# Performance work log

Measured on AMD Instinct MI355X. Metric: run time of the kernel, lower is better.

Reference implementation:

```python
import jax, jax.numpy as jnp
import numpy as np

NA, NB = 4096, 4096
IN, H, E = 256, 512, 131072
NEG_SLOPE = 0.2


def setup_inputs() -> dict:
    key = jax.random.key(0)
    ks = jax.random.split(key, 32)
    f32 = jnp.float32
    nrm = lambda k, s, sc=0.05: jax.random.normal(k, s, f32) * sc
    inp = {
        'x_A': jax.random.normal(ks[0], (NA, IN), f32),
        'x_B': jax.random.normal(ks[1], (NB, IN), f32),
        'edge_AB': jax.random.randint(ks[2], (2, E), 0, NA, jnp.int32),
        'edge_BA': jax.random.randint(ks[3], (2, E), 0, NB, jnp.int32),
        'W_inA': nrm(ks[4], (H, IN)), 'b_inA': jnp.zeros((H,), f32),
        'W_inB': nrm(ks[5], (H, IN)), 'b_inB': jnp.zeros((H,), f32),
        'W_in2A': nrm(ks[6], (H, IN)), 'b_in2A': jnp.zeros((H,), f32),
        'W_in2B': nrm(ks[7], (H, IN)), 'b_in2B': jnp.zeros((H,), f32),
        'Wg1': nrm(ks[8], (H, H)), 'a_src1': nrm(ks[9], (H,)),
        'a_dst1': nrm(ks[10], (H,)), 'bg1': jnp.zeros((H,), f32),
        'Wg2': nrm(ks[11], (H, H)), 'a_src2': nrm(ks[12], (H,)),
        'a_dst2': nrm(ks[13], (H,)), 'bg2': jnp.zeros((H,), f32),
        'Wqkv': nrm(ks[14], (3 * H, H)), 'bqkv': jnp.zeros((3 * H,), f32),
        'Wo': nrm(ks[15], (H, H)), 'bo': jnp.zeros((H,), f32),
    }
    return inp


def gat_conv(x, src, dst, W, a_src, a_dst, b, n):
    # PyG GATConv, heads=1: linear transform, per-edge additive attention,
    # LeakyReLU + segment softmax over incoming edges of each dst node,
    # scatter-sum of weighted source messages. Self-loops already in src/dst.
    h = x @ W.T                                # [n, H]
    e = jax.nn.leaky_relu((h @ a_src)[src] + (h @ a_dst)[dst], NEG_SLOPE)
    m = jax.ops.segment_max(e, dst, num_segments=n)
    ex = jnp.exp(e - m[dst])
    denom = jax.ops.segment_sum(ex, dst, num_segments=n)
    alpha = ex / denom[dst]                    # [E']
    out = jax.ops.segment_sum(h[src] * alpha[:, None], dst, num_segments=n)
    return out + b


def reference(x_A, x_B, edge_AB, edge_BA, W_inA, b_inA, W_inB, b_inB,
              W_in2A, b_in2A, W_in2B, b_in2B,
              Wg1, a_src1, a_dst1, bg1, Wg2, a_src2, a_dst2, bg2,
              Wqkv, bqkv, Wo, bo):
    na, nb = x_A.shape[0], x_B.shape[0]
    n = na + nb
    l = jnp.concatenate([x_A @ W_inA.T + b_inA, x_B @ W_inB.T + b_inB], 0)
    loops = jnp.arange(n, dtype=edge_AB.dtype)
    # to_homogeneous offsets: A at 0, B at na; add self-loops (PyG default)
    src = jnp.concatenate([edge_AB[0], edge_BA[0] + na, loops])
    dst = jnp.concatenate([edge_AB[1] + na, edge_BA[1], loops])
    l = gat_conv(l, src, dst, Wg1, a_src1, a_dst1, bg1, n)
    l = gat_conv(l, src, dst, Wg2, a_src2, a_dst2, bg2, n)
    # global branch: per-type linear -> dense single-head self-attention over all nodes
    g = jnp.concatenate([x_A @ W_in2A.T + b_in2A, x_B @ W_in2B.T + b_in2B], 0)
    qkv = g @ Wqkv.T + bqkv
    q, k, v = jnp.split(qkv, 3, axis=-1)       # each [n, H]
    scale = 1.0 / jnp.sqrt(jnp.asarray(q.shape[-1], q.dtype))
    attn = jax.nn.softmax((q @ k.T) * scale, axis=-1)  # [n, n]
    g = (attn @ v) @ Wo.T + bo
    z_A = jnp.concatenate([l[:na], g[:na]], axis=1)    # [na, 2H]
    z_B = jnp.concatenate([l[na:], g[na:]], axis=1)    # [nb, 2H]
    return (z_A, z_B)
```

## Files before the change

kernel.cpp:

```cpp
#include <hip/hip_runtime.h>
#include <hip/hip_bf16.h>

#define NA_ 4096
#define NB_ 4096
#define NN_ 8192
#define EE_ 131072
#define NE_ (2*EE_ + NN_)
#define HH_ 512
#define NEG_SLOPE_ 0.2f

typedef __attribute__((ext_vector_type(4))) float f32x4;
typedef __attribute__((ext_vector_type(8))) short s16x8;

__device__ inline unsigned short f2bf(float v) {
    __hip_bfloat16 h = __float2bfloat16(v);
    return __builtin_bit_cast(unsigned short, h);
}
__device__ inline float bf2f(unsigned short u) {
    return __uint_as_float(((unsigned)u) << 16);
}

__device__ inline unsigned fkey(float f) {
    unsigned b = __float_as_uint(f);
    return (b & 0x80000000u) ? ~b : (b | 0x80000000u);
}
__device__ inline float finv(unsigned k) {
    return (k & 0x80000000u) ? __uint_as_float(k & 0x7fffffffu)
                             : __uint_as_float(~k);
}

__device__ inline void edge_sd(int i, const int* __restrict__ eAB,
                               const int* __restrict__ eBA, int& s, int& d) {
    if (i < EE_)            { s = eAB[i];            d = eAB[EE_ + i] + NA_; }
    else if (i < 2 * EE_)   { int j = i - EE_; s = eBA[j] + NA_; d = eBA[EE_ + j]; }
    else                    { s = i - 2 * EE_;       d = s; }
}

struct CvtJob { const float* s; unsigned short* hi; unsigned short* lo; int n4; };
struct CvtJobs { CvtJob j[10]; };

__global__ __launch_bounds__(256) void cvt_all_k(CvtJobs jobs) {
    const CvtJob jb = jobs.j[blockIdx.y];
    int i = blockIdx.x * 256 + threadIdx.x;
    if (i >= jb.n4) return;
    float4 v = ((const float4*)jb.s)[i];
    ushort4 h;
    h.x = f2bf(v.x); h.y = f2bf(v.y); h.z = f2bf(v.z); h.w = f2bf(v.w);
    ((ushort4*)jb.hi)[i] = h;
    if (jb.lo) {
        ushort4 l;
        l.x = f2bf(v.x - bf2f(h.x));
        l.y = f2bf(v.y - bf2f(h.y));
        l.z = f2bf(v.z - bf2f(h.z));
        l.w = f2bf(v.w - bf2f(h.w));
        ((ushort4*)jb.lo)[i] = l;
    }
}

template<int BM, int BN, bool BIAS, typename OutT>
__global__ __launch_bounds__(256) void mgemm_k(
    const unsigned short* __restrict__ A, const unsigned short* __restrict__ B,
    const float* __restrict__ bias, OutT* __restrict__ C,
    int K, int lda, int ldb, int ldc)
{
    constexpr int BK = 32;
    constexpr int WM = BM / 2, WN = BN / 2;
    constexpr int AM = WM / 16, AN = WN / 16;
    constexpr int AISS = BM * 4 / 256, BISS = BN * 4 / 256;
    __shared__ unsigned short sA[BM * BK];
    __shared__ unsigned short sB[BN * BK];
    const int t = threadIdx.x, lane = t & 63, w = t >> 6;
    const int wr = w >> 1, wc = w & 1;
    const int fr = lane & 15, fq = lane >> 4;
    const int bm = blockIdx.y * BM, bn = blockIdx.x * BN;

    f32x4 acc[AM][AN];
    #pragma unroll
    for (int m = 0; m < AM; m++)
        #pragma unroll
        for (int n = 0; n < AN; n++)
            #pragma unroll
            for (int r = 0; r < 4; r++) acc[m][n][r] = 0.f;

    for (int k0 = 0; k0 < K; k0 += BK) {
        __syncthreads();
        #pragma unroll
        for (int i = 0; i < AISS; i++) {
            int slot = i * 256 + t;
            __builtin_amdgcn_global_load_lds(
                (const __attribute__((address_space(1))) unsigned int*)
                    (A + (size_t)(bm + (slot >> 2)) * lda + k0 + (slot & 3) * 8),
                (__attribute__((address_space(3))) unsigned int*)
                    (sA + (i * 256 + w * 64) * 8), 16, 0, 0);
        }
        #pragma unroll
        for (int i = 0; i < BISS; i++) {
            int slot = i * 256 + t;
            __builtin_amdgcn_global_load_lds(
                (const __attribute__((address_space(1))) unsigned int*)
                    (B + (size_t)(bn + (slot >> 2)) * ldb + k0 + (slot & 3) * 8),
                (__attribute__((address_space(3))) unsigned int*)
                    (sB + (i * 256 + w * 64) * 8), 16, 0, 0);
        }
        __syncthreads();
        s16x8 a[AM], b[AN];
        #pragma unroll
        for (int m = 0; m < AM; m++)
            a[m] = *(const s16x8*)&sA[(wr * WM + m * 16 + fr) * BK + fq * 8];
        #pragma unroll
        for (int n = 0; n < AN; n++)
            b[n] = *(const s16x8*)&sB[(wc * WN + n * 16 + fr) * BK + fq * 8];
        #pragma unroll
        for (int m = 0; m < AM; m++)
            #pragma unroll
            for (int n = 0; n < AN; n++)
                acc[m][n] = __builtin_amdgcn_mfma_f32_16x16x32_bf16(a[m], b[n], acc[m][n], 0, 0, 0);
    }

    #pragma unroll
    for (int m = 0; m < AM; m++) {
        const int row = bm + wr * WM + m * 16 + fq * 4;
        #pragma unroll
        for (int n = 0; n < AN; n++) {
            const int col = bn + wc * WN + n * 16 + fr;
            const float bv = BIAS ? bias[col] : 0.f;
            #pragma unroll
            for (int r = 0; r < 4; r++) {
                float v = acc[m][n][r] + bv;
                if constexpr (sizeof(OutT) == 2)
                    C[(size_t)(row + r) * ldc + col] = (OutT)f2bf(v);
                else
                    C[(size_t)(row + r) * ldc + col] = v;
            }
        }
    }
}

__global__ __launch_bounds__(512) void mgemm_qk_k(
    const unsigned short* __restrict__ A, const unsigned short* __restrict__ B,
    unsigned short* __restrict__ C, float* __restrict__ denom)
{
    constexpr int BK = 64;
    __shared__ unsigned short sA[256 * BK];
    __shared__ unsigned short sB[256 * BK];
    const int t = threadIdx.x, lane = t & 63, w = t >> 6;
    const int wr = w >> 2, wc = w & 3;
    const int fr = lane & 15, fq = lane >> 4;
    const int bm = blockIdx.y * 256, bn = blockIdx.x * 256;

    f32x4 acc[8][4];
    #pragma unroll
    for (int m = 0; m < 8; m++)
        #pragma unroll
        for (int n = 0; n < 4; n++)
            #pragma unroll
            for (int r = 0; r < 4; r++) acc[m][n][r] = 0.f;

    for (int k0 = 0; k0 < 512; k0 += BK) {
        __syncthreads();
        #pragma unroll
        for (int i = 0; i < 4; i++) {
            int s = i * 512 + t;
            int row = s >> 3, cc = s & 7;
            int gc = k0 + ((cc ^ (row & 7)) << 3);
            __builtin_amdgcn_global_load_lds(
                (const __attribute__((address_space(1))) unsigned int*)
                    (A + (size_t)(bm + row) * 512 + gc),
                (__attribute__((address_space(3))) unsigned int*)
                    (sA + (i * 512 + w * 64) * 8), 16, 0, 0);
            __builtin_amdgcn_global_load_lds(
                (const __attribute__((address_space(1))) unsigned int*)
                    (B + (size_t)(bn + row) * 512 + gc),
                (__attribute__((address_space(3))) unsigned int*)
                    (sB + (i * 512 + w * 64) * 8), 16, 0, 0);
        }
        __syncthreads();
        #pragma unroll
        for (int kk = 0; kk < 2; kk++) {
            s16x8 a[8], b[4];
            #pragma unroll
            for (int m = 0; m < 8; m++) {
                int row = wr * 128 + m * 16 + fr;
                a[m] = *(const s16x8*)&sA[row * BK + (((kk * 4 + fq) ^ (row & 7)) << 3)];
            }
            #pragma unroll
            for (int n = 0; n < 4; n++) {
                int row = wc * 64 + n * 16 + fr;
                b[n] = *(const s16x8*)&sB[row * BK + (((kk * 4 + fq) ^ (row & 7)) << 3)];
            }
            #pragma unroll
            for (int m = 0; m < 8; m++)
                #pragma unroll
                for (int n = 0; n < 4; n++)
                    acc[m][n] = __builtin_amdgcn_mfma_f32_16x16x32_bf16(a[m], b[n], acc[m][n], 0, 0, 0);
        }
    }

    #pragma unroll
    for (int m = 0; m < 8; m++) {
        #pragma unroll
        for (int r = 0; r < 4; r++) {
            const int row = bm + wr * 128 + m * 16 + fq * 4 + r;
            float rsum = 0.f;
            #pragma unroll
            for (int n = 0; n < 4; n++) {
                const int col = bn + wc * 64 + n * 16 + fr;
                float p = exp2f(acc[m][n][r]);
                rsum += p;
                C[(size_t)row * 8192 + col] = f2bf(p);
            }
            rsum += __shfl_xor(rsum, 1);
            rsum += __shfl_xor(rsum, 2);
            rsum += __shfl_xor(rsum, 4);
            rsum += __shfl_xor(rsum, 8);
            if (fr == 0) atomicAdd(&denom[row], rsum);
        }
    }
}

template<bool SPLIT>
__global__ __launch_bounds__(256) void mgemm_in_k(
    const unsigned short* __restrict__ xA, const unsigned short* __restrict__ xB,
    const unsigned short* __restrict__ WA, const unsigned short* __restrict__ WB,
    const float* __restrict__ biasA, const float* __restrict__ biasB,
    unsigned short* __restrict__ o1, unsigned short* __restrict__ o2)
{
    constexpr int BK = 32;
    __shared__ unsigned short sA[128 * BK];
    __shared__ unsigned short sB[128 * BK];
    const int t = threadIdx.x, lane = t & 63, w = t >> 6;
    const int wr = w >> 1, wc = w & 1;
    const int fr = lane & 15, fq = lane >> 4;
    const int bm = blockIdx.y * 128, bn = blockIdx.x * 128;
    const bool isB = bm >= NA_;
    const unsigned short* A = isB ? xB : xA;
    const unsigned short* W = isB ? WB : WA;
    const float* bias = isB ? biasB : biasA;
    const int bml = bm - (isB ? NA_ : 0);

    f32x4 acc[4][4];
    #pragma unroll
    for (int m = 0; m < 4; m++)
        #pragma unroll
        for (int n = 0; n < 4; n++)
            #pragma unroll
            for (int r = 0; r < 4; r++) acc[m][n][r] = 0.f;

    for (int k0 = 0; k0 < 256; k0 += BK) {
        __syncthreads();
        #pragma unroll
        for (int i = 0; i < 2; i++) {
            int slot = i * 256 + t;
            __builtin_amdgcn_global_load_lds(
                (const __attribute__((address_space(1))) unsigned int*)
                    (A + (size_t)(bml + (slot >> 2)) * 256 + k0 + (slot & 3) * 8),
                (__attribute__((address_space(3))) unsigned int*)
                    (sA + (i * 256 + w * 64) * 8), 16, 0, 0);
            __builtin_amdgcn_global_load_lds(
                (const __attribute__((address_space(1))) unsigned int*)
                    (W + (size_t)(bn + (slot >> 2)) * 256 + k0 + (slot & 3) * 8),
                (__attribute__((address_space(3))) unsigned int*)
                    (sB + (i * 256 + w * 64) * 8), 16, 0, 0);
        }
        __syncthreads();
        s16x8 a[4], b[4];
        #pragma unroll
        for (int m = 0; m < 4; m++)
            a[m] = *(const s16x8*)&sA[(wr * 64 + m * 16 + fr) * BK + fq * 8];
        #pragma unroll
        for (int n = 0; n < 4; n++)
            b[n] = *(const s16x8*)&sB[(wc * 64 + n * 16 + fr) * BK + fq * 8];
        #pragma unroll
        for (int m = 0; m < 4; m++)
            #pragma unroll
            for (int n = 0; n < 4; n++)
                acc[m][n] = __builtin_amdgcn_mfma_f32_16x16x32_bf16(a[m], b[n], acc[m][n], 0, 0, 0);
    }

    #pragma unroll
    for (int m = 0; m < 4; m++) {
        const int row = bm + wr * 64 + m * 16 + fq * 4;
        #pragma unroll
        for (int n = 0; n < 4; n++) {
            const int col = bn + wc * 64 + n * 16 + fr;
            const float bv = bias[col];
            #pragma unroll
            for (int r = 0; r < 4; r++) {
                float v = acc[m][n][r] + bv;
                unsigned short hi = f2bf(v);
                o1[(size_t)(row + r) * 512 + col] = hi;
                if (SPLIT)
                    o2[(size_t)(row + r) * 512 + col] = f2bf(v - bf2f(hi));
            }
        }
    }
}

__global__ __launch_bounds__(256) void mgemm3_k(
    const unsigned short* __restrict__ Ahi, const unsigned short* __restrict__ Alo,
    const unsigned short* __restrict__ Bhi, const unsigned short* __restrict__ Blo,
    unsigned short* __restrict__ Cb, int K, int lda, int ldb)
{
    constexpr int BM = 128, BN = 128, BK = 32;
    __shared__ unsigned short sAh[BM * BK], sAl[BM * BK];
    __shared__ unsigned short sBh[BN * BK], sBl[BN * BK];
    const int t = threadIdx.x, lane = t & 63, w = t >> 6;
    const int wr = w >> 1, wc = w & 1;
    const int fr = lane & 15, fq = lane >> 4;
    const int bm = blockIdx.y * BM, bn = blockIdx.x * BN;

    f32x4 acc[4][4];
    #pragma unroll
    for (int m = 0; m < 4; m++)
        #pragma unroll
        for (int n = 0; n < 4; n++)
            #pragma unroll
            for (int r = 0; r < 4; r++) acc[m][n][r] = 0.f;

    for (int k0 = 0; k0 < K; k0 += BK) {
        __syncthreads();
        #pragma unroll
        for (int i = 0; i < 2; i++) {
            int slot = i * 256 + t;
            size_t ga = (size_t)(bm + (slot >> 2)) * lda + k0 + (slot & 3) * 8;
            size_t gb = (size_t)(bn + (slot >> 2)) * ldb + k0 + (slot & 3) * 8;
            unsigned loff = (unsigned)(i * 256 + w * 64) * 8;
            __builtin_amdgcn_global_load_lds(
                (const __attribute__((address_space(1))) unsigned int*)(Ahi + ga),
                (__attribute__((address_space(3))) unsigned int*)(sAh + loff), 16, 0, 0);
            __builtin_amdgcn_global_load_lds(
                (const __attribute__((address_space(1))) unsigned int*)(Alo + ga),
                (__attribute__((address_space(3))) unsigned int*)(sAl + loff), 16, 0, 0);
            __builtin_amdgcn_global_load_lds(
                (const __attribute__((address_space(1))) unsigned int*)(Bhi + gb),
                (__attribute__((address_space(3))) unsigned int*)(sBh + loff), 16, 0, 0);
            __builtin_amdgcn_global_load_lds(
                (const __attribute__((address_space(1))) unsigned int*)(Blo + gb),
                (__attribute__((address_space(3))) unsigned int*)(sBl + loff), 16, 0, 0);
        }
        __syncthreads();
        s16x8 ah[4], al[4], bh[4], bl[4];
        #pragma unroll
        for (int m = 0; m < 4; m++) {
            int o = (wr * 64 + m * 16 + fr) * BK + fq * 8;
            ah[m] = *(const s16x8*)&sAh[o];
            al[m] = *(const s16x8*)&sAl[o];
        }
        #pragma unroll
        for (int n = 0; n < 4; n++) {
            int o = (wc * 64 + n * 16 + fr) * BK + fq * 8;
            bh[n] = *(const s16x8*)&sBh[o];
            bl[n] = *(const s16x8*)&sBl[o];
        }
        #pragma unroll
        for (int m = 0; m < 4; m++)
            #pragma unroll
            for (int n = 0; n < 4; n++) {
                acc[m][n] = __builtin_amdgcn_mfma_f32_16x16x32_bf16(ah[m], bh[n], acc[m][n], 0, 0, 0);
                acc[m][n] = __builtin_amdgcn_mfma_f32_16x16x32_bf16(ah[m], bl[n], acc[m][n], 0, 0, 0);
                acc[m][n] = __builtin_amdgcn_mfma_f32_16x16x32_bf16(al[m], bh[n], acc[m][n], 0, 0, 0);
            }
    }

    #pragma unroll
    for (int m = 0; m < 4; m++) {
        const int row = bm + wr * 64 + m * 16 + fq * 4;
        #pragma unroll
        for (int n = 0; n < 4; n++) {
            const int col = bn + wc * 64 + n * 16 + fr;
            #pragma unroll
            for (int r = 0; r < 4; r++)
                Cb[(size_t)(row + r) * 512 + col] = f2bf(acc[m][n][r]);
        }
    }
}

__global__ __launch_bounds__(256) void mgemm_pv_k(
    const unsigned short* __restrict__ A, const unsigned short* __restrict__ B,
    unsigned short* __restrict__ C, int kseg, size_t segstride)
{
    constexpr int BK = 64;
    __shared__ unsigned short sA[128 * BK];
    __shared__ unsigned short sB[128 * BK];
    const int t = threadIdx.x, lane = t & 63, w = t >> 6;
    const int wr = w >> 1, wc = w & 1;
    const int fr = lane & 15, fq = lane >> 4;
    const int L  = blockIdx.x + (blockIdx.y << 2) + (blockIdx.z << 6);
    const int xs = L >> 7;
    const int ys = (L & 127) & 15;
    const int zs = (L & 127) >> 4;
    const int bm = ys * 128, bn = xs * 128;
    const int kofs = zs * kseg;

    f32x4 acc[4][4];
    #pragma unroll
    for (int m = 0; m < 4; m++)
        #pragma unroll
        for (int n = 0; n < 4; n++)
            #pragma unroll
            for (int r = 0; r < 4; r++) acc[m][n][r] = 0.f;

    for (int k0 = 0; k0 < kseg; k0 += BK) {
        __syncthreads();
        #pragma unroll
        for (int i = 0; i < 4; i++) {
            int s = i * 256 + t;
            int row = s >> 3, cc = s & 7;
            int gc = kofs + k0 + ((cc ^ (row & 7)) << 3);
            __builtin_amdgcn_global_load_lds(
                (const __attribute__((address_space(1))) unsigned int*)
                    (A + (size_t)(bm + row) * 8192 + gc),
                (__attribute__((address_space(3))) unsigned int*)
                    (sA + (i * 256 + w * 64) * 8), 16, 0, 0);
            __builtin_amdgcn_global_load_lds(
                (const __attribute__((address_space(1))) unsigned int*)
                    (B + (size_t)(bn + row) * 8192 + gc),
                (__attribute__((address_space(3))) unsigned int*)
                    (sB + (i * 256 + w * 64) * 8), 16, 0, 0);
        }
        __syncthreads();
        #pragma unroll
        for (int kk = 0; kk < 2; kk++) {
            s16x8 a[4], b[4];
            #pragma unroll
            for (int m = 0; m < 4; m++) {
                int row = wr * 64 + m * 16 + fr;
                a[m] = *(const s16x8*)&sA[row * BK + (((kk * 4 + fq) ^ (row & 7)) << 3)];
            }
            #pragma unroll
            for (int n = 0; n < 4; n++) {
                int row = wc * 64 + n * 16 + fr;
                b[n] = *(const s16x8*)&sB[row * BK + (((kk * 4 + fq) ^ (row & 7)) << 3)];
            }
            #pragma unroll
            for (int m = 0; m < 4; m++)
                #pragma unroll
                for (int n = 0; n < 4; n++)
                    acc[m][n] = __builtin_amdgcn_mfma_f32_16x16x32_bf16(a[m], b[n], acc[m][n], 0, 0, 0);
        }
    }

    unsigned short* Cz = C + (size_t)zs * segstride;
    #pragma unroll
    for (int m = 0; m < 4; m++) {
        const int row = bm + wr * 64 + m * 16 + fq * 4;
        #pragma unroll
        for (int n = 0; n < 4; n++) {
            const int col = bn + wc * 64 + n * 16 + fr;
            #pragma unroll
            for (int r = 0; r < 4; r++)
                Cz[(size_t)(row + r) * 512 + col] = f2bf(acc[m][n][r]);
        }
    }
}

__global__ __launch_bounds__(256) void radd_k(const unsigned short* __restrict__ src,
                                              unsigned short* __restrict__ dst,
                                              const float* __restrict__ dn,
                                              int n8, int segs, size_t stride8) {
    int i = blockIdx.x * 256 + threadIdx.x;
    if (i >= n8) return;
    float acc[8] = {0,0,0,0,0,0,0,0};
    for (int s = 0; s < segs; s++) {
        s16x8 v = ((const s16x8*)src)[i + s * stride8];
        #pragma unroll
        for (int j = 0; j < 8; j++) acc[j] += bf2f((unsigned short)v[j]);
    }
    const float rd = 1.0f / dn[i >> 6];
    s16x8 o;
    #pragma unroll
    for (int j = 0; j < 8; j++) o[j] = (short)f2bf(acc[j] * rd);
    ((s16x8*)dst)[i] = o;
}

__global__ __launch_bounds__(256) void mgemm_qkv_k(
    const unsigned short* __restrict__ A, const unsigned short* __restrict__ B,
    const float* __restrict__ bias, float scale,
    unsigned short* __restrict__ qb, unsigned short* __restrict__ kb,
    unsigned short* __restrict__ vb)
{
    constexpr int BM = 128, BN = 128, BK = 32;
    __shared__ unsigned short sA[BM * BK];
    __shared__ unsigned short sB[BN * BK];
    const int t = threadIdx.x, lane = t & 63, w = t >> 6;
    const int wr = w >> 1, wc = w & 1;
    const int fr = lane & 15, fq = lane >> 4;
    const int bm = blockIdx.y * BM, bn = blockIdx.x * BN;

    f32x4 acc[4][4];
    #pragma unroll
    for (int m = 0; m < 4; m++)
        #pragma unroll
        for (int n = 0; n < 4; n++)
            #pragma unroll
            for (int r = 0; r < 4; r++) acc[m][n][r] = 0.f;

    for (int k0 = 0; k0 < 512; k0 += BK) {
        __syncthreads();
        #pragma unroll
        for (int i = 0; i < 2; i++) {
            int slot = i * 256 + t;
            __builtin_amdgcn_global_load_lds(
                (const __attribute__((address_space(1))) unsigned int*)
                    (A + (size_t)(bm + (slot >> 2)) * 512 + k0 + (slot & 3) * 8),
                (__attribute__((address_space(3))) unsigned int*)
                    (sA + (i * 256 + w * 64) * 8), 16, 0, 0);
            __builtin_amdgcn_global_load_lds(
                (const __attribute__((address_space(1))) unsigned int*)
                    (B + (size_t)(bn + (slot >> 2)) * 512 + k0 + (slot & 3) * 8),
                (__attribute__((address_space(3))) unsigned int*)
                    (sB + (i * 256 + w * 64) * 8), 16, 0, 0);
        }
        __syncthreads();
        s16x8 a[4], b[4];
        #pragma unroll
        for (int m = 0; m < 4; m++)
            a[m] = *(const s16x8*)&sA[(wr * 64 + m * 16 + fr) * BK + fq * 8];
        #pragma unroll
        for (int n = 0; n < 4; n++)
            b[n] = *(const s16x8*)&sB[(wc * 64 + n * 16 + fr) * BK + fq * 8];
        #pragma unroll
        for (int m = 0; m < 4; m++)
            #pragma unroll
            for (int n = 0; n < 4; n++)
                acc[m][n] = __builtin_amdgcn_mfma_f32_16x16x32_bf16(a[m], b[n], acc[m][n], 0, 0, 0);
    }

    #pragma unroll
    for (int m = 0; m < 4; m++) {
        const int row = bm + wr * 64 + m * 16 + fq * 4;
        #pragma unroll
        for (int n = 0; n < 4; n++) {
            const int col = bn + wc * 64 + n * 16 + fr;
            const float bv = bias[col];
            #pragma unroll
            for (int r = 0; r < 4; r++) {
                float v = acc[m][n][r] + bv;
                if (col < 512)
                    qb[(size_t)(row + r) * 512 + col] = f2bf(v * scale);
                else if (col < 1024)
                    kb[(size_t)(row + r) * 512 + (col - 512)] = f2bf(v);
                else
                    vb[(size_t)(row + r) * 512 + (col - 1024)] = f2bf(v);
            }
        }
    }
}

__global__ __launch_bounds__(256) void trT_k(const unsigned short* __restrict__ vb,
                                             unsigned short* __restrict__ vT) {
    __shared__ unsigned short s[64][65];
    const int t = threadIdx.x;
    const int rowo = blockIdx.y * 64;
    const int colo = blockIdx.x * 64;
    {
        int r = t >> 2, cg = (t & 3) * 16;
        const s16x8* src = (const s16x8*)(vb + (size_t)(rowo + r) * 512 + colo + cg);
        s16x8 u0 = src[0], u1 = src[1];
        #pragma unroll
        for (int j = 0; j < 8; j++) {
            s[r][cg + j]     = (unsigned short)u0[j];
            s[r][cg + 8 + j] = (unsigned short)u1[j];
        }
    }
    __syncthreads();
    {
        int c = t >> 2, rg = (t & 3) * 16;
        s16x8 o0, o1;
        #pragma unroll
        for (int j = 0; j < 8; j++) {
            o0[j] = (short)s[rg + j][c];
            o1[j] = (short)s[rg + 8 + j][c];
        }
        s16x8* dst = (s16x8*)(vT + (size_t)(colo + c) * 8192 + rowo + rg);
        dst[0] = o0; dst[1] = o1;
    }
}

__global__ __launch_bounds__(256) void node_dots_k(
    const unsigned short* __restrict__ hb, const float* __restrict__ a_src,
    const float* __restrict__ a_dst, float* __restrict__ as_, float* __restrict__ ad_)
{
    int wid  = (blockIdx.x * 256 + threadIdx.x) >> 6;
    int lane = threadIdx.x & 63;
    if (wid >= NN_) return;
    s16x8 hv = *(const s16x8*)(hb + (size_t)wid * HH_ + lane * 8);
    float s1 = 0.f, s2 = 0.f;
    #pragma unroll
    for (int j = 0; j < 8; j++) {
        float v = bf2f((unsigned short)hv[j]);
        s1 = fmaf(v, a_src[lane * 8 + j], s1);
        s2 = fmaf(v, a_dst[lane * 8 + j], s2);
    }
    #pragma unroll
    for (int off = 32; off; off >>= 1) {
        s1 += __shfl_down(s1, off);
        s2 += __shfl_down(s2, off);
    }
    if (lane == 0) { as_[wid] = s1; ad_[wid] = s2; }
}

__global__ void count_deg_k(const int* eAB, const int* eBA, int* deg) {
    int i = blockIdx.x * 256 + threadIdx.x;
    if (i >= NE_) return;
    int s, d; edge_sd(i, eAB, eBA, s, d);
    atomicAdd(&deg[d], 1);
}

__global__ __launch_bounds__(256) void scan_k(const int* __restrict__ deg, int* rowstart) {
    __shared__ int part[256];
    int t = threadIdx.x;
    int base = t * 32;
    int loc[32]; int s = 0;
    #pragma unroll
    for (int j = 0; j < 32; j++) { loc[j] = s; s += deg[base + j]; }
    part[t] = s;
    __syncthreads();
    if (t == 0) {
        int a = 0;
        for (int i = 0; i < 256; i++) { int v = part[i]; part[i] = a; a += v; }
        rowstart[NN_] = a;
    }
    __syncthreads();
    int off = part[t];
    #pragma unroll
    for (int j = 0; j < 32; j++) rowstart[base + j] = off + loc[j];
}

__global__ void fill_csr_k(const int* eAB, const int* eBA,
                           const int* __restrict__ rowstart, int* cursor,
                           int* csr_src, int* pos) {
    int i = blockIdx.x * 256 + threadIdx.x;
    if (i >= NE_) return;
    int s, d; edge_sd(i, eAB, eBA, s, d);
    int p = atomicAdd(&cursor[d], 1);
    int slot = rowstart[d] + p;
    csr_src[slot] = s;
    pos[i] = slot;
}

__global__ void edge_pass1_k(const int* eAB, const int* eBA,
                             const float* __restrict__ as_, const float* __restrict__ ad_,
                             float* evals, unsigned* mkey) {
    int i = blockIdx.x * 256 + threadIdx.x;
    if (i >= NE_) return;
    int s, d; edge_sd(i, eAB, eBA, s, d);
    float e = as_[s] + ad_[d];
    e = (e >= 0.f) ? e : NEG_SLOPE_ * e;
    evals[i] = e;
    atomicMax(&mkey[d], fkey(e));
}

__global__ void edge_pass2_k(const int* eAB, const int* eBA,
                             const unsigned* __restrict__ mkey,
                             const float* __restrict__ evals,
                             const int* __restrict__ pos,
                             float* __restrict__ evs, float* denom) {
    int i = blockIdx.x * 256 + threadIdx.x;
    if (i >= NE_) return;
    int s, d; edge_sd(i, eAB, eBA, s, d);
    float m = finv(mkey[d]);
    float ex = expf(evals[i] - m);
    evs[pos[i]] = ex;
    atomicAdd(&denom[d], ex);
}

template<bool SPLIT>
__global__ __launch_bounds__(256) void gat_agg_k(
    const int* __restrict__ rowstart, const int* __restrict__ csr_src,
    const float* __restrict__ evs, const float* __restrict__ denom,
    const unsigned short* __restrict__ hb, const float* __restrict__ bias,
    float* __restrict__ outF, int ldo,
    unsigned short* __restrict__ outHi, unsigned short* __restrict__ outLo)
{
    int wid  = (blockIdx.x * 256 + threadIdx.x) >> 6;
    int lane = threadIdx.x & 63;
    if (wid >= NN_) return;
    float acc[8] = {0.f,0.f,0.f,0.f,0.f,0.f,0.f,0.f};
    int beg = rowstart[wid], end = rowstart[wid + 1];
    float rden = 1.0f / denom[wid];
    for (int p = beg; p < end; p++) {
        int s = csr_src[p];
        float alpha = evs[p] * rden;
        s16x8 hv = *(const s16x8*)(hb + (size_t)s * HH_ + lane * 8);
        #pragma unroll
        for (int j = 0; j < 8; j++)
            acc[j] = fmaf(alpha, bf2f((unsigned short)hv[j]), acc[j]);
    }
    #pragma unroll
    for (int j = 0; j < 8; j++) acc[j] += bias[lane * 8 + j];
    if (SPLIT) {
        s16x8 hi, lo;
        #pragma unroll
        for (int j = 0; j < 8; j++) {
            unsigned short h = f2bf(acc[j]);
            hi[j] = (short)h;
            lo[j] = (short)f2bf(acc[j] - bf2f(h));
        }
        *(s16x8*)(outHi + (size_t)wid * HH_ + lane * 8) = hi;
        *(s16x8*)(outLo + (size_t)wid * HH_ + lane * 8) = lo;
    } else {
        float* o = outF + (size_t)wid * ldo + lane * 8;
        *(float4*)(o)     = make_float4(acc[0], acc[1], acc[2], acc[3]);
        *(float4*)(o + 4) = make_float4(acc[4], acc[5], acc[6], acc[7]);
    }
}

extern "C" void kernel_launch(void* const* d_in, const int* in_sizes, int n_in,
                              void* d_out, int out_size, void* d_ws, size_t ws_size,
                              hipStream_t stream)
{
    const float* x_A    = (const float*)d_in[0];
    const float* x_B    = (const float*)d_in[1];
    const int*   eAB    = (const int*)d_in[2];
    const int*   eBA    = (const int*)d_in[3];
    const float* W_inA  = (const float*)d_in[4];  const float* b_inA  = (const float*)d_in[5];
    const float* W_inB  = (const float*)d_in[6];  const float* b_inB  = (const float*)d_in[7];
    const float* W_in2A = (const float*)d_in[8];  const float* b_in2A = (const float*)d_in[9];
    const float* W_in2B = (const float*)d_in[10]; const float* b_in2B = (const float*)d_in[11];
    const float* Wg1    = (const float*)d_in[12]; const float* a_src1 = (const float*)d_in[13];
    const float* a_dst1 = (const float*)d_in[14]; const float* bg1    = (const float*)d_in[15];
    const float* Wg2    = (const float*)d_in[16]; const float* a_src2 = (const float*)d_in[17];
    const float* a_dst2 = (const float*)d_in[18]; const float* bg2    = (const float*)d_in[19];
    const float* Wqkv   = (const float*)d_in[20]; const float* bqkv   = (const float*)d_in[21];
    const float* Wo     = (const float*)d_in[22]; const float* bo     = (const float*)d_in[23];

    float* out = (float*)d_out;

    char* base = (char*)d_ws;
    size_t off = 0;
    auto alloc = [&](size_t nb) -> char* {
        char* p = base + off;
        off = (off + nb + 255) & ~(size_t)255;
        return p;
    };

    float*          bufA  = (float*)alloc((size_t)NN_ * 512 * 4);
    float*          bufB  = (float*)alloc((size_t)NN_ * 512 * 4);
    float*          bufC  = (float*)alloc((size_t)NN_ * 512 * 4);
    float*          as_   = (float*)alloc(NN_ * 4);
    float*          ad_   = (float*)alloc(NN_ * 4);
    unsigned*       mkey  = (unsigned*)alloc(NN_ * 4);
    float*          denom = (float*)alloc(NN_ * 4);
    int*            deg   = (int*)alloc(NN_ * 4);
    int*            cursor= (int*)alloc(NN_ * 4);
    float*          cdn   = (float*)alloc(NN_ * 4);
    int*            rowst = (int*)alloc((NN_ + 1) * 4);
    float*          evals = (float*)alloc((size_t)NE_ * 4);
    int*            csrs  = (int*)alloc((size_t)NE_ * 4);
    int*            pos   = (int*)alloc((size_t)NE_ * 4);
    float*          evs   = (float*)alloc((size_t)NE_ * 4);
    unsigned short* xbA   = (unsigned short*)alloc((size_t)NA_ * 256 * 2);
    unsigned short* xbB   = (unsigned short*)alloc((size_t)NB_ * 256 * 2);
    unsigned short* WbinA = (unsigned short*)alloc((size_t)512 * 256 * 2);
    unsigned short* WbinB = (unsigned short*)alloc((size_t)512 * 256 * 2);
    unsigned short* Wbin2A= (unsigned short*)alloc((size_t)512 * 256 * 2);
    unsigned short* Wbin2B= (unsigned short*)alloc((size_t)512 * 256 * 2);
    unsigned short* Wbqkv = (unsigned short*)alloc((size_t)1536 * 512 * 2);
    unsigned short* Wbo   = (unsigned short*)alloc((size_t)512 * 512 * 2);
    unsigned short* Wg1hi = (unsigned short*)alloc((size_t)512 * 512 * 2);
    unsigned short* Wg1lo = (unsigned short*)alloc((size_t)512 * 512 * 2);
    unsigned short* Wg2hi = (unsigned short*)alloc((size_t)512 * 512 * 2);
    unsigned short* Wg2lo = (unsigned short*)alloc((size_t)512 * 512 * 2);
    unsigned short* qb    = (unsigned short*)alloc((size_t)NN_ * 512 * 2);
    unsigned short* kb    = (unsigned short*)alloc((size_t)NN_ * 512 * 2);
    unsigned short* vT    = (unsigned short*)alloc((size_t)512 * NN_ * 2);
    unsigned short* ab    = (unsigned short*)alloc((size_t)NN_ * 512 * 2);

    unsigned short* hb = vT;
    unsigned short* gb = (unsigned short*)bufC;
    unsigned short* vb = gb + (size_t)NN_ * 512;
    unsigned short* Sb = (unsigned short*)bufA;
    unsigned short* pv = (unsigned short*)bufC;

    const int R = 2048, SEGS = 8, KSEG = 8192 / SEGS;
    const int EG = (NE_ + 255) / 256;
    const float scale2 = 0.044194173824159216f * 1.4426950408889634f;

    CvtJobs jobs;
    jobs.j[0] = { x_A,    xbA,    nullptr, NA_ * 256 / 4 };
    jobs.j[1] = { x_B,    xbB,    nullptr, NB_ * 256 / 4 };
    jobs.j[2] = { W_inA,  WbinA,  nullptr, 512 * 256 / 4 };
    jobs.j[3] = { W_inB,  WbinB,  nullptr, 512 * 256 / 4 };
    jobs.j[4] = { W_in2A, Wbin2A, nullptr, 512 * 256 / 4 };
    jobs.j[5] = { W_in2B, Wbin2B, nullptr, 512 * 256 / 4 };
    jobs.j[6] = { Wqkv,   Wbqkv,  nullptr, 1536 * 512 / 4 };
    jobs.j[7] = { Wo,     Wbo,    nullptr, 512 * 512 / 4 };
    jobs.j[8] = { Wg1,    Wg1hi,  Wg1lo,   512 * 512 / 4 };
    jobs.j[9] = { Wg2,    Wg2hi,  Wg2lo,   512 * 512 / 4 };
    cvt_all_k<<<dim3(NA_ * 256 / 4 / 256, 10), 256, 0, stream>>>(jobs);

    hipMemsetAsync(mkey, 0, (size_t)NN_ * 4 * 5, stream);

    count_deg_k<<<EG, 256, 0, stream>>>(eAB, eBA, deg);
    scan_k<<<1, 256, 0, stream>>>(deg, rowst);
    fill_csr_k<<<EG, 256, 0, stream>>>(eAB, eBA, rowst, cursor, csrs, pos);

    mgemm_in_k<true><<<dim3(4, 64), 256, 0, stream>>>(
        xbA, xbB, WbinA, WbinB, b_inA, b_inB, qb, kb);
    mgemm3_k<<<dim3(4, 64), 256, 0, stream>>>(qb, kb, Wg1hi, Wg1lo,
                                              hb, 512, 512, 512);
    node_dots_k<<<NN_/4, 256, 0, stream>>>(hb, a_src1, a_dst1, as_, ad_);
    edge_pass1_k<<<EG, 256, 0, stream>>>(eAB, eBA, as_, ad_, evals, mkey);
    edge_pass2_k<<<EG, 256, 0, stream>>>(eAB, eBA, mkey, evals, pos, evs, denom);
    gat_agg_k<true><<<NN_/4, 256, 0, stream>>>(rowst, csrs, evs, denom,
                                               hb, bg1, nullptr, 0, qb, kb);
    mgemm3_k<<<dim3(4, 64), 256, 0, stream>>>(qb, kb, Wg2hi, Wg2lo,
                                              hb, 512, 512, 512);
    node_dots_k<<<NN_/4, 256, 0, stream>>>(hb, a_src2, a_dst2, as_, ad_);
    hipMemsetAsync(mkey, 0, NN_ * 8, stream);
    edge_pass1_k<<<EG, 256, 0, stream>>>(eAB, eBA, as_, ad_, evals, mkey);
    edge_pass2_k<<<EG, 256, 0, stream>>>(eAB, eBA, mkey, evals, pos, evs, denom);
    gat_agg_k<false><<<NN_/4, 256, 0, stream>>>(rowst, csrs, evs, denom,
                                                hb, bg2, out, 1024, nullptr, nullptr);

    mgemm_in_k<false><<<dim3(4, 64), 256, 0, stream>>>(
        xbA, xbB, Wbin2A, Wbin2B, b_in2A, b_in2B, gb, nullptr);
    mgemm_qkv_k<<<dim3(12, 64), 256, 0, stream>>>(gb, Wbqkv, bqkv, scale2, qb, kb, vb);
    trT_k<<<dim3(8, 128), 256, 0, stream>>>(vb, vT);
    for (int c0 = 0; c0 < 8192; c0 += R) {
        float* dn = cdn + c0;
        mgemm_qk_k<<<dim3(32, 8), 512, 0, stream>>>(
            qb + (size_t)c0 * 512, kb, Sb, dn);
        mgemm_pv_k<<<dim3(4, R/128, SEGS), 256, 0, stream>>>(
            Sb, vT, pv, KSEG, (size_t)R * 512);
        radd_k<<<(R*512/8 + 255)/256, 256, 0, stream>>>(
            pv, ab + (size_t)c0 * 512, dn, R*512/8, SEGS, (size_t)R*512/8);
    }
    mgemm_k<128,128,true,float><<<dim3(4, 64), 256, 0, stream>>>(
        ab, Wbo, bo, out + 512, 512, 512, 512, 1024);
}
```

Measured before the change: 611.4 us.

## Stage QK epilogue through LDS for coalesced stores; fuse attention dots into GAT GEMM

The QK GEMM epilogue now writes exp2 probabilities into a padded shared-memory tile in four row chunks, then stores them as 16-byte vectors per row, replacing scattered 2-byte global writes. The GAT linear GEMM also computes the per-node a_src/a_dst dot products from its fp32 accumulators and reduces them into as_/ad_ with atomics, removing the separate node_dots kernel and its re-read of hb. This adds memsets to zero as_/ad_ (the buffers are assumed contiguous with mkey) plus extra barriers in the epilogue. The dot products now come from fp32 values rather than bf16-rounded ones, and atomic ordering makes them nondeterministic.

Result: no change. 603.8 us (-1.2%).

```diff
diff --git a/kernel.cpp b/kernel.cpp
--- a/kernel.cpp
+++ b/kernel.cpp
@@ -141,8 +141,10 @@
     unsigned short* __restrict__ C, float* __restrict__ denom)
 {
     constexpr int BK = 64;
-    __shared__ unsigned short sA[256 * BK];
-    __shared__ unsigned short sB[256 * BK];
+    __shared__ unsigned short smem[32768];
+    unsigned short* sA = smem;
+    unsigned short* sB = smem + 16384;
+    unsigned short* tile = smem;
     const int t = threadIdx.x, lane = t & 63, w = t >> 6;
     const int wr = w >> 2, wc = w & 3;
     const int fr = lane & 15, fq = lane >> 4;
@@ -197,23 +199,37 @@
     }
 
     #pragma unroll
-    for (int m = 0; m < 8; m++) {
-        #pragma unroll
-        for (int r = 0; r < 4; r++) {
-            const int row = bm + wr * 128 + m * 16 + fq * 4 + r;
-            float rsum = 0.f;
-            #pragma unroll
-            for (int n = 0; n < 4; n++) {
-                const int col = bn + wc * 64 + n * 16 + fr;
-                float p = exp2f(acc[m][n][r]);
-                rsum += p;
-                C[(size_t)row * 8192 + col] = f2bf(p);
-            }
-            rsum += __shfl_xor(rsum, 1);
-            rsum += __shfl_xor(rsum, 2);
-            rsum += __shfl_xor(rsum, 4);
-            rsum += __shfl_xor(rsum, 8);
-            if (fr == 0) atomicAdd(&denom[row], rsum);
+    for (int h = 0; h < 4; h++) {
+        __syncthreads();
+        #pragma unroll
+        for (int mm = 0; mm < 2; mm++) {
+            const int m = h * 2 + mm;
+            #pragma unroll
+            for (int r = 0; r < 4; r++) {
+                float rsum = 0.f;
+                #pragma unroll
+                for (int n = 0; n < 4; n++) {
+                    float p = exp2f(acc[m][n][r]);
+                    rsum += p;
+                    tile[(wr * 32 + mm * 16 + fq * 4 + r) * 264 + wc * 64 + n * 16 + fr]
+                        = f2bf(p);
+                }
+                rsum += __shfl_xor(rsum, 1);
+                rsum += __shfl_xor(rsum, 2);
+                rsum += __shfl_xor(rsum, 4);
+                rsum += __shfl_xor(rsum, 8);
+                if (fr == 0)
+                    atomicAdd(&denom[bm + wr * 128 + h * 32 + mm * 16 + fq * 4 + r], rsum);
+            }
+        }
+        __syncthreads();
+        #pragma unroll
+        for (int j = 0; j < 4; j++) {
+            int cj = j * 512 + t;
+            int row_l = cj >> 5, c16 = cj & 31;
+            int grow = bm + (row_l >> 5) * 128 + h * 32 + (row_l & 31);
+            *(s16x8*)(C + (size_t)grow * 8192 + bn + c16 * 8)
+                = *(const s16x8*)&tile[row_l * 264 + c16 * 8];
         }
     }
 }
@@ -299,7 +315,9 @@
 __global__ __launch_bounds__(256) void mgemm3_k(
     const unsigned short* __restrict__ Ahi, const unsigned short* __restrict__ Alo,
     const unsigned short* __restrict__ Bhi, const unsigned short* __restrict__ Blo,
-    unsigned short* __restrict__ Cb, int K, int lda, int ldb)
+    unsigned short* __restrict__ Cb, const float* __restrict__ a_src,
+    const float* __restrict__ a_dst, float* __restrict__ as_,
+    float* __restrict__ ad_, int K, int lda, int ldb)
 {
     constexpr int BM = 128, BN = 128, BK = 32;
     __shared__ unsigned short sAh[BM * BK], sAl[BM * BK];
@@ -362,15 +380,36 @@
             }
     }
 
+    float asv[4], adv[4];
+    #pragma unroll
+    for (int n = 0; n < 4; n++) {
+        const int col = bn + wc * 64 + n * 16 + fr;
+        asv[n] = a_src[col];
+        adv[n] = a_dst[col];
+    }
+
     #pragma unroll
     for (int m = 0; m < 4; m++) {
         const int row = bm + wr * 64 + m * 16 + fq * 4;
         #pragma unroll
-        for (int n = 0; n < 4; n++) {
-            const int col = bn + wc * 64 + n * 16 + fr;
-            #pragma unroll
-            for (int r = 0; r < 4; r++)
-                Cb[(size_t)(row + r) * 512 + col] = f2bf(acc[m][n][r]);
+        for (int r = 0; r < 4; r++) {
+            float s1 = 0.f, s2 = 0.f;
+            #pragma unroll
+            for (int n = 0; n < 4; n++) {
+                const int col = bn + wc * 64 + n * 16 + fr;
+                float v = acc[m][n][r];
+                Cb[(size_t)(row + r) * 512 + col] = f2bf(v);
+                s1 = fmaf(v, asv[n], s1);
+                s2 = fmaf(v, adv[n], s2);
+            }
+            s1 += __shfl_xor(s1, 1); s2 += __shfl_xor(s2, 1);
+            s1 += __shfl_xor(s1, 2); s2 += __shfl_xor(s2, 2);
+            s1 += __shfl_xor(s1, 4); s2 += __shfl_xor(s2, 4);
+            s1 += __shfl_xor(s1, 8); s2 += __shfl_xor(s2, 8);
+            if (fr == 0) {
+                atomicAdd(&as_[row + r], s1);
+                atomicAdd(&ad_[row + r], s2);
+            }
         }
     }
 }
@@ -575,29 +614,6 @@
         s16x8* dst = (s16x8*)(vT + (size_t)(colo + c) * 8192 + rowo + rg);
         dst[0] = o0; dst[1] = o1;
     }
-}
-
-__global__ __launch_bounds__(256) void node_dots_k(
-    const unsigned short* __restrict__ hb, const float* __restrict__ a_src,
-    const float* __restrict__ a_dst, float* __restrict__ as_, float* __restrict__ ad_)
-{
-    int wid  = (blockIdx.x * 256 + threadIdx.x) >> 6;
-    int lane = threadIdx.x & 63;
-    if (wid >= NN_) return;
-    s16x8 hv = *(const s16x8*)(hb + (size_t)wid * HH_ + lane * 8);
-    float s1 = 0.f, s2 = 0.f;
-    #pragma unroll
-    for (int j = 0; j < 8; j++) {
-        float v = bf2f((unsigned short)hv[j]);
-        s1 = fmaf(v, a_src[lane * 8 + j], s1);
-        s2 = fmaf(v, a_dst[lane * 8 + j], s2);
-    }
-    #pragma unroll
-    for (int off = 32; off; off >>= 1) {
-        s1 += __shfl_down(s1, off);
-        s2 += __shfl_down(s2, off);
-    }
-    if (lane == 0) { as_[wid] = s1; ad_[wid] = s2; }
 }
 
 __global__ void count_deg_k(const int* eAB, const int* eBA, int* deg) {
@@ -790,7 +806,7 @@
     jobs.j[9] = { Wg2,    Wg2hi,  Wg2lo,   512 * 512 / 4 };
     cvt_all_k<<<dim3(NA_ * 256 / 4 / 256, 10), 256, 0, stream>>>(jobs);
 
-    hipMemsetAsync(mkey, 0, (size_t)NN_ * 4 * 5, stream);
+    hipMemsetAsync(as_, 0, (size_t)NN_ * 4 * 7, stream);
 
     count_deg_k<<<EG, 256, 0, stream>>>(eAB, eBA, deg);
     scan_k<<<1, 256, 0, stream>>>(deg, rowst);
@@ -799,16 +815,16 @@
     mgemm_in_k<true><<<dim3(4, 64), 256, 0, stream>>>(
         xbA, xbB, WbinA, WbinB, b_inA, b_inB, qb, kb);
     mgemm3_k<<<dim3(4, 64), 256, 0, stream>>>(qb, kb, Wg1hi, Wg1lo,
-                                              hb, 512, 512, 512);
-    node_dots_k<<<NN_/4, 256, 0, stream>>>(hb, a_src1, a_dst1, as_, ad_);
+                                              hb, a_src1, a_dst1, as_, ad_,
+                                              512, 512, 512);
     edge_pass1_k<<<EG, 256, 0, stream>>>(eAB, eBA, as_, ad_, evals, mkey);
     edge_pass2_k<<<EG, 256, 0, stream>>>(eAB, eBA, mkey, evals, pos, evs, denom);
     gat_agg_k<true><<<NN_/4, 256, 0, stream>>>(rowst, csrs, evs, denom,
                                                hb, bg1, nullptr, 0, qb, kb);
+    hipMemsetAsync(as_, 0, NN_ * 16, stream);
     mgemm3_k<<<dim3(4, 64), 256, 0, stream>>>(qb, kb, Wg2hi, Wg2lo,
-                                              hb, 512, 512, 512);
-    node_dots_k<<<NN_/4, 256, 0, stream>>>(hb, a_src2, a_dst2, as_, ad_);
-    hipMemsetAsync(mkey, 0, NN_ * 8, stream);
+                                              hb, a_src2, a_dst2, as_, ad_,
+                                              512, 512, 512);
     edge_pass1_k<<<EG, 256, 0, stream>>>(eAB, eBA, as_, ad_, evals, mkey);
     edge_pass2_k<<<EG, 256, 0, stream>>>(eAB, eBA, mkey, evals, pos, evs, denom);
     gat_agg_k<false><<<NN_/4, 256, 0, stream>>>(rowst, csrs, evs, denom,
```
